# Optimization experiments

Hardware: AMD Instinct MI355X
Metric: run time of the kernel (lower is better)

## Reference

```python
import jax, jax.numpy as jnp
import numpy as np

B, D, O, E, H, K = 4096, 1024, 1024, 8, 4096, 2


def setup_inputs() -> dict:
    key = jax.random.key(0)
    ks = jax.random.split(key, 5)
    scale_g = 1.0 / np.sqrt(D)
    scale_1 = 1.0 / np.sqrt(D)
    scale_2 = 1.0 / np.sqrt(H)
    return {
        "x": jax.random.normal(ks[0], (B, D), jnp.float32),
        "gate_w": jax.random.normal(ks[1], (D, E), jnp.float32) * scale_g,
        "gate_b": jnp.zeros((E,), jnp.float32),
        "w1": jax.random.normal(ks[2], (E, D, H), jnp.float32) * scale_1,
        "b1": jnp.zeros((E, H), jnp.float32),
        "w2": jax.random.normal(ks[3], (E, H, O), jnp.float32) * scale_2,
        "b2": jnp.zeros((E, O), jnp.float32),
    }


def reference(x, gate_w, gate_b, w1, b1, w2, b2):
    # Router: top-k logits, softmax over the k selected logits only
    logits = x @ gate_w + gate_b                      # [B, E]
    top_vals, top_idx = jax.lax.top_k(logits, K)      # [B, K]
    routing_w = jax.nn.softmax(top_vals, axis=-1)     # [B, K]

    # Dense all-expert MLP (grouped GEMM), then gather the k selected outputs
    h = jax.nn.relu(jnp.einsum("bd,edh->beh", x, w1) + b1)  # [B, E, H]
    y = jnp.einsum("beh,eho->beo", h, w2) + b2              # [B, E, O]
    sel = jnp.take_along_axis(y, top_idx[:, :, None], axis=1)  # [B, K, O]
    return jnp.sum(routing_w[:, :, None] * sel, axis=1)        # [B, O]
```

## Files before the change

kernel.cpp:

```cpp
#include <hip/hip_runtime.h>
#include <stdint.h>

typedef short bf16x8 __attribute__((ext_vector_type(8)));
typedef float f32x4  __attribute__((ext_vector_type(4)));

constexpr int BT = 4096;
constexpr int DD = 1024;
constexpr int OO = 1024;
constexpr int EE = 8;
constexpr int HH = 4096;
constexpr int SLOTS = 2 * BT;

__device__ __forceinline__ unsigned short f2bf(float f) {
  unsigned u = __float_as_uint(f);
  u += 0x7fffu + ((u >> 16) & 1u);
  return (unsigned short)(u >> 16);
}

__device__ __forceinline__ void glds16(const unsigned short* g, unsigned short* l) {
  __builtin_amdgcn_global_load_lds(
      (const __attribute__((address_space(1))) void*)g,
      (__attribute__((address_space(3))) void*)l, 16, 0, 0);
}

__global__ __launch_bounds__(256) void router_k(const float* __restrict__ x,
                                                const float* __restrict__ gw,
                                                const float* __restrict__ gb,
                                                unsigned short* __restrict__ xb,
                                                int* __restrict__ cnt,
                                                int* __restrict__ list,
                                                float* __restrict__ rw) {
  int wave = threadIdx.x >> 6, lane = threadIdx.x & 63;
  int b = blockIdx.x * 4 + wave;
  const float* xrow = x + (size_t)b * DD;
  float acc[8];
#pragma unroll
  for (int e = 0; e < 8; ++e) acc[e] = 0.f;
#pragma unroll
  for (int i = 0; i < 4; ++i) {
    int d0 = i * 256 + lane * 4;
    float4 v = *(const float4*)&xrow[d0];
    unsigned lo = (unsigned)f2bf(v.x) | ((unsigned)f2bf(v.y) << 16);
    unsigned hi = (unsigned)f2bf(v.z) | ((unsigned)f2bf(v.w) << 16);
    *(uint2*)&xb[(size_t)b * DD + d0] = make_uint2(lo, hi);
    const float* g0 = &gw[(size_t)d0 * 8];
    float fv[4] = {v.x, v.y, v.z, v.w};
#pragma unroll
    for (int q = 0; q < 4; ++q) {
      float4 ga = *(const float4*)&g0[q * 8];
      float4 gc = *(const float4*)&g0[q * 8 + 4];
      acc[0] += fv[q] * ga.x; acc[1] += fv[q] * ga.y;
      acc[2] += fv[q] * ga.z; acc[3] += fv[q] * ga.w;
      acc[4] += fv[q] * gc.x; acc[5] += fv[q] * gc.y;
      acc[6] += fv[q] * gc.z; acc[7] += fv[q] * gc.w;
    }
  }
#pragma unroll
  for (int off = 32; off > 0; off >>= 1) {
#pragma unroll
    for (int e = 0; e < 8; ++e) acc[e] += __shfl_down(acc[e], off);
  }
  if (lane == 0) {
    float v[8];
#pragma unroll
    for (int e = 0; e < 8; ++e) v[e] = acc[e] + gb[e];
    int i0 = 0;
#pragma unroll
    for (int e = 1; e < 8; ++e) if (v[e] > v[i0]) i0 = e;
    int i1 = (i0 == 0) ? 1 : 0;
#pragma unroll
    for (int e = 0; e < 8; ++e) if (e != i0 && v[e] > v[i1]) i1 = e;
    float e1 = __expf(v[i1] - v[i0]);
    float inv = 1.0f / (1.0f + e1);
    int p0 = atomicAdd(&cnt[i0], 1);
    list[i0 * BT + p0] = 2 * b;     rw[2 * b]     = inv;
    int p1 = atomicAdd(&cnt[i1], 1);
    list[i1 * BT + p1] = 2 * b + 1; rw[2 * b + 1] = e1 * inv;
  }
}

__global__ void tilemap_k(const int* __restrict__ cnt, int* __restrict__ tmap,
                          int* __restrict__ ntiles) {
  if (threadIdx.x == 0 && blockIdx.x == 0) {
    int t = 0, basewalk = 0;
    for (int e = 0; e < EE; ++e) {
      int c = cnt[e];
      for (int m0 = 0; m0 < c; m0 += 128) {
        tmap[4 * t] = e; tmap[4 * t + 1] = m0; tmap[4 * t + 2] = basewalk + m0; ++t;
      }
      basewalk += c;
    }
    *ntiles = t;
  }
}

__global__ __launch_bounds__(256) void cvt_t_k(const float* __restrict__ src,
                                               unsigned short* __restrict__ dst,
                                               int R, int C) {
  __shared__ unsigned short tile[64][66];
  int e = blockIdx.z;
  const float* s = src + (size_t)e * R * C;
  unsigned short* d = dst + (size_t)e * R * C;
  int r0 = blockIdx.x << 6, c0 = blockIdx.y << 6;
  int t = threadIdx.x;
#pragma unroll
  for (int p = 0; p < 4; ++p) {
    int ch = p * 256 + t;
    int rr = ch >> 4, cc = (ch & 15) << 2;
    float4 v = *(const float4*)&s[(size_t)(r0 + rr) * C + c0 + cc];
    unsigned lo = (unsigned)f2bf(v.x) | ((unsigned)f2bf(v.y) << 16);
    unsigned hi = (unsigned)f2bf(v.z) | ((unsigned)f2bf(v.w) << 16);
    *(uint2*)&tile[rr][cc] = make_uint2(lo, hi);
  }
  __syncthreads();
#pragma unroll
  for (int p = 0; p < 4; ++p) {
    int ch = p * 256 + t;
    int cc = ch >> 4, rr = (ch & 15) << 2;
    unsigned short v0 = tile[rr + 0][cc];
    unsigned short v1 = tile[rr + 1][cc];
    unsigned short v2 = tile[rr + 2][cc];
    unsigned short v3 = tile[rr + 3][cc];
    unsigned lo = (unsigned)v0 | ((unsigned)v1 << 16);
    unsigned hi = (unsigned)v2 | ((unsigned)v3 << 16);
    *(uint2*)&d[(size_t)(c0 + cc) * R + r0 + rr] = make_uint2(lo, hi);
  }
}

__global__ __launch_bounds__(256, 4) void gemm1_k(const unsigned short* __restrict__ xb,
                                                  const unsigned short* __restrict__ w1t,
                                                  const float* __restrict__ b1,
                                                  const int* __restrict__ cnt,
                                                  const int* __restrict__ list,
                                                  const int* __restrict__ tmap,
                                                  const int* __restrict__ ntiles,
                                                  unsigned short* __restrict__ hc) {
  int ti = blockIdx.y;
  if (ti >= *ntiles) return;
  int e = tmap[4 * ti], m0 = tmap[4 * ti + 1], base = tmap[4 * ti + 2];
  int cnt_e = cnt[e];
  int n0 = blockIdx.x * 128;

  __shared__ int slotbuf[128];
  __shared__ __align__(16) unsigned short Ash[128 * 64];
  __shared__ __align__(16) unsigned short Bsh[128 * 64];

  int t = threadIdx.x;
  if (t < 128) {
    int r = m0 + t;
    slotbuf[t] = list[e * BT + (r < cnt_e ? r : 0)];
  }
  __syncthreads();

  int w = t >> 6, l = t & 63;
  int lm = l & 15, lq = l >> 4;
  int wm = (w & 1) * 64, wn = (w >> 1) * 64;

  const unsigned short* Bsrc = w1t + (size_t)e * HH * DD + (size_t)n0 * DD;

  const unsigned short* aS[4];
  const unsigned short* bS[4];
  unsigned short* aL[4];
  unsigned short* bL[4];
#pragma unroll
  for (int j = 0; j < 4; ++j) {
    int idx = 4 * w + j;
    int row = idx * 8 + (l >> 3);
    int koff = (l & 7) * 8;
    int tok = slotbuf[row] >> 1;
    aS[j] = xb + (size_t)tok * DD + koff;
    bS[j] = Bsrc + (size_t)row * DD + koff;
    aL[j] = &Ash[idx * 512];
    bL[j] = &Bsh[idx * 512];
  }

  f32x4 acc[4][4];
#pragma unroll
  for (int mi = 0; mi < 4; ++mi)
#pragma unroll
    for (int ni = 0; ni < 4; ++ni) acc[mi][ni] = f32x4{0.f, 0.f, 0.f, 0.f};

  for (int k0 = 0; k0 < DD; k0 += 64) {
#pragma unroll
    for (int j = 0; j < 4; ++j) glds16(aS[j] + k0, aL[j]);
#pragma unroll
    for (int j = 0; j < 4; ++j) glds16(bS[j] + k0, bL[j]);
    __syncthreads();
#pragma unroll
    for (int ks = 0; ks < 2; ++ks) {
      bf16x8 af[4], bfr[4];
      int kb = ks * 32 + lq * 8;
#pragma unroll
      for (int mi = 0; mi < 4; ++mi)
        af[mi] = *(const bf16x8*)&Ash[(wm + mi * 16 + lm) * 64 + kb];
#pragma unroll
      for (int ni = 0; ni < 4; ++ni)
        bfr[ni] = *(const bf16x8*)&Bsh[(wn + ni * 16 + lm) * 64 + kb];
#pragma unroll
      for (int mi = 0; mi < 4; ++mi)
#pragma unroll
        for (int ni = 0; ni < 4; ++ni)
          acc[mi][ni] = __builtin_amdgcn_mfma_f32_16x16x32_bf16(af[mi], bfr[ni], acc[mi][ni], 0, 0, 0);
    }
    __syncthreads();
  }

#pragma unroll
  for (int ni = 0; ni < 4; ++ni) {
    int ncol = n0 + wn + ni * 16 + lm;
    float bias = b1[e * HH + ncol];
#pragma unroll
    for (int mi = 0; mi < 4; ++mi) {
      int mbase = wm + mi * 16 + lq * 4;
#pragma unroll
      for (int r = 0; r < 4; ++r) {
        int mrow = mbase + r;
        if (m0 + mrow < cnt_e) {
          float v = fmaxf(acc[mi][ni][r] + bias, 0.0f);
          hc[(size_t)(base + mrow) * HH + ncol] = f2bf(v);
        }
      }
    }
  }
}

__global__ __launch_bounds__(256, 4) void gemm2_k(const unsigned short* __restrict__ hc,
                                                  const unsigned short* __restrict__ w2t,
                                                  const float* __restrict__ b2,
                                                  const int* __restrict__ cnt,
                                                  const int* __restrict__ list,
                                                  const int* __restrict__ tmap,
                                                  const int* __restrict__ ntiles,
                                                  const float* __restrict__ rw,
                                                  float* __restrict__ ybuf,
                                                  float* __restrict__ out) {
  int ti = blockIdx.y;
  if (ti >= *ntiles) return;
  int e = tmap[4 * ti], m0 = tmap[4 * ti + 1], base = tmap[4 * ti + 2];
  int cnt_e = cnt[e];
  int n0 = blockIdx.x * 128;
  int ksl = HH / gridDim.z;
  int kb0 = blockIdx.z * ksl;

  __shared__ int slotbuf[128];
  __shared__ float rwbuf[128];
  __shared__ __align__(16) unsigned short Ash[128 * 64];
  __shared__ __align__(16) unsigned short Bsh[128 * 64];

  int t = threadIdx.x;
  if (t < 128) {
    int r = m0 + t;
    int s_ = list[e * BT + (r < cnt_e ? r : 0)];
    slotbuf[t] = s_;
    rwbuf[t] = rw[s_];
  }
  __syncthreads();

  int w = t >> 6, l = t & 63;
  int lm = l & 15, lq = l >> 4;
  int wm = (w & 1) * 64, wn = (w >> 1) * 64;

  const unsigned short* Bsrc = w2t + (size_t)e * OO * HH + (size_t)n0 * HH;

  const unsigned short* aS[4];
  const unsigned short* bS[4];
  unsigned short* aL[4];
  unsigned short* bL[4];
#pragma unroll
  for (int j = 0; j < 4; ++j) {
    int idx = 4 * w + j;
    int row = idx * 8 + (l >> 3);
    int koff = (l & 7) * 8;
    aS[j] = hc + (size_t)(base + row) * HH + kb0 + koff;
    bS[j] = Bsrc + (size_t)row * HH + kb0 + koff;
    aL[j] = &Ash[idx * 512];
    bL[j] = &Bsh[idx * 512];
  }

  f32x4 acc[4][4];
#pragma unroll
  for (int mi = 0; mi < 4; ++mi)
#pragma unroll
    for (int ni = 0; ni < 4; ++ni) acc[mi][ni] = f32x4{0.f, 0.f, 0.f, 0.f};

  for (int k0 = 0; k0 < ksl; k0 += 64) {
#pragma unroll
    for (int j = 0; j < 4; ++j) glds16(aS[j] + k0, aL[j]);
#pragma unroll
    for (int j = 0; j < 4; ++j) glds16(bS[j] + k0, bL[j]);
    __syncthreads();
#pragma unroll
    for (int ks = 0; ks < 2; ++ks) {
      bf16x8 af[4], bfr[4];
      int kb = ks * 32 + lq * 8;
#pragma unroll
      for (int mi = 0; mi < 4; ++mi)
        af[mi] = *(const bf16x8*)&Ash[(wm + mi * 16 + lm) * 64 + kb];
#pragma unroll
      for (int ni = 0; ni < 4; ++ni)
        bfr[ni] = *(const bf16x8*)&Bsh[(wn + ni * 16 + lm) * 64 + kb];
#pragma unroll
      for (int mi = 0; mi < 4; ++mi)
#pragma unroll
        for (int ni = 0; ni < 4; ++ni)
          acc[mi][ni] = __builtin_amdgcn_mfma_f32_16x16x32_bf16(af[mi], bfr[ni], acc[mi][ni], 0, 0, 0);
    }
    __syncthreads();
  }

  bool addbias = (blockIdx.z == 0);
  size_t ybase = (size_t)blockIdx.z * SLOTS;
#pragma unroll
  for (int ni = 0; ni < 4; ++ni) {
    int ncol = n0 + wn + ni * 16 + lm;
    float bias = addbias ? b2[e * OO + ncol] : 0.0f;
#pragma unroll
    for (int mi = 0; mi < 4; ++mi) {
      int mbase = wm + mi * 16 + lq * 4;
#pragma unroll
      for (int r = 0; r < 4; ++r) {
        int mrow = mbase + r;
        if (m0 + mrow < cnt_e) {
          float v = (acc[mi][ni][r] + bias) * rwbuf[mrow];
          int slot = slotbuf[mrow];
          if (ybuf) ybuf[(ybase + slot) * OO + ncol] = v;
          else      atomicAdd(&out[(size_t)(slot >> 1) * OO + ncol], v);
        }
      }
    }
  }
}

__global__ __launch_bounds__(256) void combine_k(const float* __restrict__ y,
                                                 float* __restrict__ out, int nz) {
  int i = blockIdx.x * 256 + threadIdx.x;
  int b = i >> 8, c = i & 255;
  f32x4 acc = {0.f, 0.f, 0.f, 0.f};
  for (int z = 0; z < nz; ++z) {
#pragma unroll
    for (int k = 0; k < 2; ++k) {
      const float4 v = *(const float4*)&y[((size_t)z * SLOTS + 2 * b + k) * OO + c * 4];
      acc[0] += v.x; acc[1] += v.y; acc[2] += v.z; acc[3] += v.w;
    }
  }
  *(f32x4*)&out[(size_t)b * OO + c * 4] = acc;
}

extern "C" void kernel_launch(void* const* d_in, const int* in_sizes, int n_in,
                              void* d_out, int out_size, void* d_ws, size_t ws_size,
                              hipStream_t stream) {
  const float* x  = (const float*)d_in[0];
  const float* gw = (const float*)d_in[1];
  const float* gb = (const float*)d_in[2];
  const float* w1 = (const float*)d_in[3];
  const float* b1 = (const float*)d_in[4];
  const float* w2 = (const float*)d_in[5];
  const float* b2 = (const float*)d_in[6];
  float* out = (float*)d_out;
  char* ws = (char*)d_ws;

  int*            cnt    = (int*)(ws);
  int*            ntiles = (int*)(ws + 64);
  int*            tmap   = (int*)(ws + 128);
  float*          rw     = (float*)(ws + 4096);
  int*            list   = (int*)(ws + (64u << 10));
  unsigned short* xb     = (unsigned short*)(ws + (1u  << 20));
  unsigned short* wt     = (unsigned short*)(ws + (9u  << 20));
  unsigned short* hc     = (unsigned short*)(ws + (73u << 20));
  float*          ybuf   = (float*)(ws + (138u << 20));

  size_t need_min = (138u << 20);
  if (ws_size < need_min) return;
  int zsplit;
  float* ypass;
  if (ws_size >= (138u << 20) + (size_t)2 * SLOTS * OO * 4) { zsplit = 2; ypass = ybuf; }
  else if (ws_size >= (138u << 20) + (size_t)SLOTS * OO * 4) { zsplit = 1; ypass = ybuf; }
  else { zsplit = 2; ypass = nullptr; }

  hipMemsetAsync(cnt, 0, 64, stream);
  if (!ypass) hipMemsetAsync(out, 0, (size_t)BT * OO * sizeof(float), stream);

  router_k<<<BT / 4, 256, 0, stream>>>(x, gw, gb, xb, cnt, list, rw);
  tilemap_k<<<1, 64, 0, stream>>>(cnt, tmap, ntiles);
  cvt_t_k<<<dim3(DD / 64, HH / 64, EE), 256, 0, stream>>>(w1, wt, DD, HH);
  gemm1_k<<<dim3(HH / 128, 72), 256, 0, stream>>>(xb, wt, b1, cnt, list, tmap, ntiles, hc);
  cvt_t_k<<<dim3(HH / 64, OO / 64, EE), 256, 0, stream>>>(w2, wt, HH, OO);
  gemm2_k<<<dim3(OO / 128, 72, zsplit), 256, 0, stream>>>(hc, wt, b2, cnt, list, tmap, ntiles, rw, ypass, out);
  if (ypass)
    combine_k<<<BT * OO / 1024, 256, 0, stream>>>(ybuf, out, zsplit);
}
```

Measured before the change: 715.7 us.

## Restructure expert GEMMs with 256x128 tiles, 4-stage LDS ring and LDS-staged stores

Both grouped GEMMs move to 512-thread blocks computing 256x128 tiles with BK=32, fed by a 4-deep ring of async global-to-LDS loads. A single barrier per k-step with vmcnt-based waits replaces the old load/sync/compute/sync pattern, and MFMA issue is given raised priority. gemm1 also stages its bf16 output through LDS for 16-byte coalesced stores. The aim is to hide memory latency and raise operand reuse per block, at the cost of more LDS, fewer blocks per CU and a tighter tile-count bound (MAXT=40).

```diff
diff --git a/kernel.cpp b/kernel.cpp
--- a/kernel.cpp
+++ b/kernel.cpp
@@ -10,6 +10,12 @@
 constexpr int EE = 8;
 constexpr int HH = 4096;
 constexpr int SLOTS = 2 * BT;
+
+constexpr int BM = 256, BN = 128, BK = 32;
+constexpr int RING = 4;
+constexpr int A_USH = BM * BK;
+constexpr int TILE_USH = (BM + BN) * BK;
+constexpr int MAXT = 40;
 
 __device__ __forceinline__ unsigned short f2bf(float f) {
   unsigned u = __float_as_uint(f);
@@ -85,7 +91,7 @@
     int t = 0, basewalk = 0;
     for (int e = 0; e < EE; ++e) {
       int c = cnt[e];
-      for (int m0 = 0; m0 < c; m0 += 128) {
+      for (int m0 = 0; m0 < c; m0 += BM) {
         tmap[4 * t] = e; tmap[4 * t + 1] = m0; tmap[4 * t + 2] = basewalk + m0; ++t;
       }
       basewalk += c;
@@ -127,7 +133,7 @@
   }
 }
 
-__global__ __launch_bounds__(256, 4) void gemm1_k(const unsigned short* __restrict__ xb,
+__global__ __launch_bounds__(512, 2) void gemm1_k(const unsigned short* __restrict__ xb,
                                                   const unsigned short* __restrict__ w1t,
                                                   const float* __restrict__ b1,
                                                   const int* __restrict__ cnt,
@@ -139,40 +145,33 @@
   if (ti >= *ntiles) return;
   int e = tmap[4 * ti], m0 = tmap[4 * ti + 1], base = tmap[4 * ti + 2];
   int cnt_e = cnt[e];
-  int n0 = blockIdx.x * 128;
-
-  __shared__ int slotbuf[128];
-  __shared__ __align__(16) unsigned short Ash[128 * 64];
-  __shared__ __align__(16) unsigned short Bsh[128 * 64];
+  int n0 = blockIdx.x * BN;
+
+  __shared__ int slotbuf[BM];
+  __shared__ __align__(16) unsigned short lds[RING * TILE_USH];
 
   int t = threadIdx.x;
-  if (t < 128) {
+  if (t < BM) {
     int r = m0 + t;
     slotbuf[t] = list[e * BT + (r < cnt_e ? r : 0)];
   }
   __syncthreads();
 
-  int w = t >> 6, l = t & 63;
-  int lm = l & 15, lq = l >> 4;
-  int wm = (w & 1) * 64, wn = (w >> 1) * 64;
-
-  const unsigned short* Bsrc = w1t + (size_t)e * HH * DD + (size_t)n0 * DD;
-
-  const unsigned short* aS[4];
-  const unsigned short* bS[4];
-  unsigned short* aL[4];
-  unsigned short* bL[4];
-#pragma unroll
-  for (int j = 0; j < 4; ++j) {
-    int idx = 4 * w + j;
-    int row = idx * 8 + (l >> 3);
-    int koff = (l & 7) * 8;
-    int tok = slotbuf[row] >> 1;
-    aS[j] = xb + (size_t)tok * DD + koff;
-    bS[j] = Bsrc + (size_t)row * DD + koff;
-    aL[j] = &Ash[idx * 512];
-    bL[j] = &Bsh[idx * 512];
-  }
+  int w = t >> 6, l = t & 63, lm = l & 15, lq = l >> 4;
+  int wr = w >> 1, wc = w & 1;
+
+  int rstage = t >> 2;
+  int ch8 = (t & 3) * 8;
+  const unsigned short* aS0 = xb + (size_t)(slotbuf[rstage] >> 1) * DD + ch8;
+  const unsigned short* aS1 = xb + (size_t)(slotbuf[128 + rstage] >> 1) * DD + ch8;
+  const unsigned short* bS  = w1t + (size_t)e * HH * DD + (size_t)(n0 + rstage) * DD + ch8;
+  int dA0 = w * 512, dA1 = 4096 + w * 512, dB = A_USH + w * 512;
+
+  int afo[4], bfo[4];
+#pragma unroll
+  for (int mi = 0; mi < 4; ++mi) afo[mi] = (wr * 64 + mi * 16 + lm) * BK + lq * 8;
+#pragma unroll
+  for (int ni = 0; ni < 4; ++ni) bfo[ni] = A_USH + (wc * 64 + ni * 16 + lm) * BK + lq * 8;
 
   f32x4 acc[4][4];
 #pragma unroll
@@ -180,51 +179,74 @@
 #pragma unroll
     for (int ni = 0; ni < 4; ++ni) acc[mi][ni] = f32x4{0.f, 0.f, 0.f, 0.f};
 
-  for (int k0 = 0; k0 < DD; k0 += 64) {
-#pragma unroll
-    for (int j = 0; j < 4; ++j) glds16(aS[j] + k0, aL[j]);
-#pragma unroll
-    for (int j = 0; j < 4; ++j) glds16(bS[j] + k0, bL[j]);
-    __syncthreads();
-#pragma unroll
-    for (int ks = 0; ks < 2; ++ks) {
-      bf16x8 af[4], bfr[4];
-      int kb = ks * 32 + lq * 8;
-#pragma unroll
-      for (int mi = 0; mi < 4; ++mi)
-        af[mi] = *(const bf16x8*)&Ash[(wm + mi * 16 + lm) * 64 + kb];
+  constexpr int NT = DD / BK;
+
+#pragma unroll
+  for (int p = 0; p < RING - 1; ++p) {
+    unsigned short* Lb = lds + p * TILE_USH;
+    glds16(aS0 + p * BK, Lb + dA0);
+    glds16(aS1 + p * BK, Lb + dA1);
+    glds16(bS  + p * BK, Lb + dB);
+  }
+  asm volatile("s_waitcnt vmcnt(6)" ::: "memory");
+  __builtin_amdgcn_s_barrier();
+  asm volatile("" ::: "memory");
+
+  for (int tt = 0; tt < NT; ++tt) {
+    const unsigned short* Lc = lds + (tt & 3) * TILE_USH;
+    bf16x8 af[4], bf[4];
+#pragma unroll
+    for (int mi = 0; mi < 4; ++mi) af[mi] = *(const bf16x8*)&Lc[afo[mi]];
+#pragma unroll
+    for (int ni = 0; ni < 4; ++ni) bf[ni] = *(const bf16x8*)&Lc[bfo[ni]];
+    {
+      int ts = tt + 3;
+      int ko = (ts < NT ? ts : NT - 1) * BK;
+      unsigned short* Lb = lds + (ts & 3) * TILE_USH;
+      glds16(aS0 + ko, Lb + dA0);
+      glds16(aS1 + ko, Lb + dA1);
+      glds16(bS  + ko, Lb + dB);
+    }
+    __builtin_amdgcn_s_setprio(1);
+#pragma unroll
+    for (int mi = 0; mi < 4; ++mi)
 #pragma unroll
       for (int ni = 0; ni < 4; ++ni)
-        bfr[ni] = *(const bf16x8*)&Bsh[(wn + ni * 16 + lm) * 64 + kb];
-#pragma unroll
-      for (int mi = 0; mi < 4; ++mi)
-#pragma unroll
-        for (int ni = 0; ni < 4; ++ni)
-          acc[mi][ni] = __builtin_amdgcn_mfma_f32_16x16x32_bf16(af[mi], bfr[ni], acc[mi][ni], 0, 0, 0);
-    }
-    __syncthreads();
-  }
-
-#pragma unroll
-  for (int ni = 0; ni < 4; ++ni) {
-    int ncol = n0 + wn + ni * 16 + lm;
-    float bias = b1[e * HH + ncol];
-#pragma unroll
-    for (int mi = 0; mi < 4; ++mi) {
-      int mbase = wm + mi * 16 + lq * 4;
-#pragma unroll
-      for (int r = 0; r < 4; ++r) {
-        int mrow = mbase + r;
-        if (m0 + mrow < cnt_e) {
-          float v = fmaxf(acc[mi][ni][r] + bias, 0.0f);
-          hc[(size_t)(base + mrow) * HH + ncol] = f2bf(v);
-        }
-      }
-    }
-  }
-}
-
-__global__ __launch_bounds__(256, 4) void gemm2_k(const unsigned short* __restrict__ hc,
+        acc[mi][ni] = __builtin_amdgcn_mfma_f32_16x16x32_bf16(af[mi], bf[ni], acc[mi][ni], 0, 0, 0);
+    __builtin_amdgcn_s_setprio(0);
+    asm volatile("s_waitcnt vmcnt(6)" ::: "memory");
+    __builtin_amdgcn_s_barrier();
+    asm volatile("" ::: "memory");
+  }
+
+  asm volatile("s_waitcnt vmcnt(0)" ::: "memory");
+  __builtin_amdgcn_s_barrier();
+  asm volatile("" ::: "memory");
+  unsigned short* cb = lds + w * 4096;
+  float bias[4];
+#pragma unroll
+  for (int ni = 0; ni < 4; ++ni) bias[ni] = b1[e * HH + n0 + wc * 64 + ni * 16 + lm];
+#pragma unroll
+  for (int mi = 0; mi < 4; ++mi)
+#pragma unroll
+    for (int ni = 0; ni < 4; ++ni)
+#pragma unroll
+      for (int r = 0; r < 4; ++r)
+        cb[(mi * 16 + lq * 4 + r) * 64 + ni * 16 + lm] =
+            f2bf(fmaxf(acc[mi][ni][r] + bias[ni], 0.0f));
+  asm volatile("s_waitcnt lgkmcnt(0)" ::: "memory");
+#pragma unroll
+  for (int it = 0; it < 8; ++it) {
+    int rr = it * 8 + (l >> 3), chk = l & 7;
+    int lrow = wr * 64 + rr;
+    if (m0 + lrow < cnt_e) {
+      uint4 v = *(const uint4*)&cb[rr * 64 + chk * 8];
+      *(uint4*)&hc[(size_t)(base + lrow) * HH + n0 + wc * 64 + chk * 8] = v;
+    }
+  }
+}
+
+__global__ __launch_bounds__(512, 2) void gemm2_k(const unsigned short* __restrict__ hc,
                                                   const unsigned short* __restrict__ w2t,
                                                   const float* __restrict__ b2,
                                                   const int* __restrict__ cnt,
@@ -238,17 +260,18 @@
   if (ti >= *ntiles) return;
   int e = tmap[4 * ti], m0 = tmap[4 * ti + 1], base = tmap[4 * ti + 2];
   int cnt_e = cnt[e];
-  int n0 = blockIdx.x * 128;
+  int n0 = blockIdx.x * BN;
+  int z = blockIdx.z;
   int ksl = HH / gridDim.z;
-  int kb0 = blockIdx.z * ksl;
-
-  __shared__ int slotbuf[128];
-  __shared__ float rwbuf[128];
-  __shared__ __align__(16) unsigned short Ash[128 * 64];
-  __shared__ __align__(16) unsigned short Bsh[128 * 64];
+  int kb0 = z * ksl;
+  int NT = ksl / BK;
+
+  __shared__ int slotbuf[BM];
+  __shared__ float rwbuf[BM];
+  __shared__ __align__(16) unsigned short lds[RING * TILE_USH];
 
   int t = threadIdx.x;
-  if (t < 128) {
+  if (t < BM) {
     int r = m0 + t;
     int s_ = list[e * BT + (r < cnt_e ? r : 0)];
     slotbuf[t] = s_;
@@ -256,26 +279,22 @@
   }
   __syncthreads();
 
-  int w = t >> 6, l = t & 63;
-  int lm = l & 15, lq = l >> 4;
-  int wm = (w & 1) * 64, wn = (w >> 1) * 64;
-
-  const unsigned short* Bsrc = w2t + (size_t)e * OO * HH + (size_t)n0 * HH;
-
-  const unsigned short* aS[4];
-  const unsigned short* bS[4];
-  unsigned short* aL[4];
-  unsigned short* bL[4];
-#pragma unroll
-  for (int j = 0; j < 4; ++j) {
-    int idx = 4 * w + j;
-    int row = idx * 8 + (l >> 3);
-    int koff = (l & 7) * 8;
-    aS[j] = hc + (size_t)(base + row) * HH + kb0 + koff;
-    bS[j] = Bsrc + (size_t)row * HH + kb0 + koff;
-    aL[j] = &Ash[idx * 512];
-    bL[j] = &Bsh[idx * 512];
-  }
+  int w = t >> 6, l = t & 63, lm = l & 15, lq = l >> 4;
+  int wr = w >> 1, wc = w & 1;
+
+  int rstage = t >> 2, ch8 = (t & 3) * 8;
+  int gr0 = base + rstage;       if (gr0 > SLOTS - 1) gr0 = SLOTS - 1;
+  int gr1 = base + 128 + rstage; if (gr1 > SLOTS - 1) gr1 = SLOTS - 1;
+  const unsigned short* aS0 = hc + (size_t)gr0 * HH + kb0 + ch8;
+  const unsigned short* aS1 = hc + (size_t)gr1 * HH + kb0 + ch8;
+  const unsigned short* bS  = w2t + (size_t)e * OO * HH + (size_t)(n0 + rstage) * HH + kb0 + ch8;
+  int dA0 = w * 512, dA1 = 4096 + w * 512, dB = A_USH + w * 512;
+
+  int afo[4], bfo[4];
+#pragma unroll
+  for (int mi = 0; mi < 4; ++mi) afo[mi] = (wr * 64 + mi * 16 + lm) * BK + lq * 8;
+#pragma unroll
+  for (int ni = 0; ni < 4; ++ni) bfo[ni] = A_USH + (wc * 64 + ni * 16 + lm) * BK + lq * 8;
 
   f32x4 acc[4][4];
 #pragma unroll
@@ -283,51 +302,62 @@
 #pragma unroll
     for (int ni = 0; ni < 4; ++ni) acc[mi][ni] = f32x4{0.f, 0.f, 0.f, 0.f};
 
-  for (int k0 = 0; k0 < ksl; k0 += 64) {
-#pragma unroll
-    for (int j = 0; j < 4; ++j) glds16(aS[j] + k0, aL[j]);
-#pragma unroll
-    for (int j = 0; j < 4; ++j) glds16(bS[j] + k0, bL[j]);
-    __syncthreads();
-#pragma unroll
-    for (int ks = 0; ks < 2; ++ks) {
-      bf16x8 af[4], bfr[4];
-      int kb = ks * 32 + lq * 8;
-#pragma unroll
-      for (int mi = 0; mi < 4; ++mi)
-        af[mi] = *(const bf16x8*)&Ash[(wm + mi * 16 + lm) * 64 + kb];
+#pragma unroll
+  for (int p = 0; p < RING - 1; ++p) {
+    unsigned short* Lb = lds + p * TILE_USH;
+    glds16(aS0 + p * BK, Lb + dA0);
+    glds16(aS1 + p * BK, Lb + dA1);
+    glds16(bS  + p * BK, Lb + dB);
+  }
+  asm volatile("s_waitcnt vmcnt(6)" ::: "memory");
+  __builtin_amdgcn_s_barrier();
+  asm volatile("" ::: "memory");
+
+  for (int tt = 0; tt < NT; ++tt) {
+    const unsigned short* Lc = lds + (tt & 3) * TILE_USH;
+    bf16x8 af[4], bf[4];
+#pragma unroll
+    for (int mi = 0; mi < 4; ++mi) af[mi] = *(const bf16x8*)&Lc[afo[mi]];
+#pragma unroll
+    for (int ni = 0; ni < 4; ++ni) bf[ni] = *(const bf16x8*)&Lc[bfo[ni]];
+    {
+      int ts = tt + 3;
+      int ko = (ts < NT ? ts : NT - 1) * BK;
+      unsigned short* Lb = lds + (ts & 3) * TILE_USH;
+      glds16(aS0 + ko, Lb + dA0);
+      glds16(aS1 + ko, Lb + dA1);
+      glds16(bS  + ko, Lb + dB);
+    }
+    __builtin_amdgcn_s_setprio(1);
+#pragma unroll
+    for (int mi = 0; mi < 4; ++mi)
 #pragma unroll
       for (int ni = 0; ni < 4; ++ni)
-        bfr[ni] = *(const bf16x8*)&Bsh[(wn + ni * 16 + lm) * 64 + kb];
-#pragma unroll
-      for (int mi = 0; mi < 4; ++mi)
-#pragma unroll
-        for (int ni = 0; ni < 4; ++ni)
-          acc[mi][ni] = __builtin_amdgcn_mfma_f32_16x16x32_bf16(af[mi], bfr[ni], acc[mi][ni], 0, 0, 0);
-    }
-    __syncthreads();
-  }
-
-  bool addbias = (blockIdx.z == 0);
-  size_t ybase = (size_t)blockIdx.z * SLOTS;
+        acc[mi][ni] = __builtin_amdgcn_mfma_f32_16x16x32_bf16(af[mi], bf[ni], acc[mi][ni], 0, 0, 0);
+    __builtin_amdgcn_s_setprio(0);
+    asm volatile("s_waitcnt vmcnt(6)" ::: "memory");
+    __builtin_amdgcn_s_barrier();
+    asm volatile("" ::: "memory");
+  }
+
+  bool addb = (z == 0);
+  size_t ybase = (size_t)z * SLOTS;
 #pragma unroll
   for (int ni = 0; ni < 4; ++ni) {
-    int ncol = n0 + wn + ni * 16 + lm;
-    float bias = addbias ? b2[e * OO + ncol] : 0.0f;
-#pragma unroll
-    for (int mi = 0; mi < 4; ++mi) {
-      int mbase = wm + mi * 16 + lq * 4;
+    int ncol = n0 + wc * 64 + ni * 16 + lm;
+    float bias = addb ? b2[e * OO + ncol] : 0.0f;
+#pragma unroll
+    for (int mi = 0; mi < 4; ++mi)
 #pragma unroll
       for (int r = 0; r < 4; ++r) {
-        int mrow = mbase + r;
-        if (m0 + mrow < cnt_e) {
-          float v = (acc[mi][ni][r] + bias) * rwbuf[mrow];
-          int slot = slotbuf[mrow];
+        int lrow = wr * 64 + mi * 16 + lq * 4 + r;
+        if (m0 + lrow < cnt_e) {
+          float v = (acc[mi][ni][r] + bias) * rwbuf[lrow];
+          int slot = slotbuf[lrow];
           if (ybuf) ybuf[(ybase + slot) * OO + ncol] = v;
           else      atomicAdd(&out[(size_t)(slot >> 1) * OO + ncol], v);
         }
       }
-    }
   }
 }
 
@@ -383,9 +413,9 @@
   router_k<<<BT / 4, 256, 0, stream>>>(x, gw, gb, xb, cnt, list, rw);
   tilemap_k<<<1, 64, 0, stream>>>(cnt, tmap, ntiles);
   cvt_t_k<<<dim3(DD / 64, HH / 64, EE), 256, 0, stream>>>(w1, wt, DD, HH);
-  gemm1_k<<<dim3(HH / 128, 72), 256, 0, stream>>>(xb, wt, b1, cnt, list, tmap, ntiles, hc);
+  gemm1_k<<<dim3(HH / BN, MAXT), 512, 0, stream>>>(xb, wt, b1, cnt, list, tmap, ntiles, hc);
   cvt_t_k<<<dim3(HH / 64, OO / 64, EE), 256, 0, stream>>>(w2, wt, HH, OO);
-  gemm2_k<<<dim3(OO / 128, 72, zsplit), 256, 0, stream>>>(hc, wt, b2, cnt, list, tmap, ntiles, rw, ypass, out);
+  gemm2_k<<<dim3(OO / BN, MAXT, zsplit), 512, 0, stream>>>(hc, wt, b2, cnt, list, tmap, ntiles, rw, ypass, out);
   if (ypass)
     combine_k<<<BT * OO / 1024, 256, 0, stream>>>(ybuf, out, zsplit);
 }
```

Result: faster. 683.2 us (-4.5%).
